# Optimization experiments

Measured on AMD Instinct MI355X. Metric: run time of the kernel, lower is better.

The kernel has to match this reference:

```python
import jax, jax.numpy as jnp
import numpy as np

B, T, C, H = 8, 1024, 1024, 16
Dh = C // H
EPS = 1e-5


def layernorm(x, g, b):
    m = jnp.mean(x, axis=-1, keepdims=True)
    v = jnp.mean((x - m) ** 2, axis=-1, keepdims=True)
    return g * (x - m) / jnp.sqrt(v + EPS) + b


def setup_inputs() -> dict:
    key = jax.random.key(0)
    ks = jax.random.split(key, 10)
    s = 0.02
    return {
        "x": jax.random.normal(ks[0], (B, T, C), jnp.float32),
        "Wq": jax.random.normal(ks[1], (H, C, Dh), jnp.float32) * s,
        "Wk": jax.random.normal(ks[2], (H, C, Dh), jnp.float32) * s,
        "Wv": jax.random.normal(ks[3], (H, C, Dh), jnp.float32) * s,
        "Wproj": jax.random.normal(ks[4], (C, C), jnp.float32) * s,
        "bproj": jnp.zeros((C,), jnp.float32),
        "W1": jax.random.normal(ks[5], (C, C), jnp.float32) * s,
        "b1": jnp.zeros((C,), jnp.float32),
        "W2": jax.random.normal(ks[6], (C, C), jnp.float32) * s,
        "b2": jnp.zeros((C,), jnp.float32),
        "g1": jnp.ones((C,), jnp.float32),
        "beta1": jnp.zeros((C,), jnp.float32),
        "g2": jnp.ones((C,), jnp.float32),
        "beta2": jnp.zeros((C,), jnp.float32),
    }


def reference(x, Wq, Wk, Wv, Wproj, bproj, W1, b1, W2, b2, g1, beta1, g2, beta2):
    # pre-LN multi-head causal self-attention + residual
    xn = layernorm(x, g1, beta1)
    q = jnp.einsum("btc,hcd->bhtd", xn, Wq)
    k = jnp.einsum("btc,hcd->bhtd", xn, Wk)
    v = jnp.einsum("btc,hcd->bhtd", xn, Wv)
    scores = jnp.einsum("bhtd,bhsd->bhts", q, k) * (Dh ** -0.5)
    causal = jnp.tril(jnp.ones((T, T), bool))  # [T,T]
    scores = jnp.where(causal, scores, -jnp.inf)
    wei = jax.nn.softmax(scores, axis=-1)
    attn = jnp.einsum("bhts,bhsd->bhtd", wei, v)
    attn = attn.transpose(0, 2, 1, 3).reshape(B, T, C)  # concat heads
    x = x + attn @ Wproj + bproj
    # pre-LN MLP (n_emb -> n_emb, ReLU, n_emb -> n_emb) + residual
    xn2 = layernorm(x, g2, beta2)
    h = jax.nn.relu(xn2 @ W1 + b1)
    x = x + h @ W2 + b2
    return x
```

## Files before the change

kernel.cpp:

```cpp
#include <hip/hip_runtime.h>
#include <hip/hip_bf16.h>

#define KDIM 1024

typedef __bf16  bf16x8  __attribute__((ext_vector_type(8)));
typedef float   floatx4 __attribute__((ext_vector_type(4)));

__device__ inline short f2bf(float f) {
    unsigned u = __float_as_uint(f);
    u += 0x7fffu + ((u >> 16) & 1u);
    return (short)(u >> 16);
}
__device__ inline float bf2f(short s) {
    return __uint_as_float(((unsigned)(unsigned short)s) << 16);
}

__device__ inline floatx4 mfma16(bf16x8 a, bf16x8 b, floatx4 c) {
    return __builtin_amdgcn_mfma_f32_16x16x32_bf16(a, b, c, 0, 0, 0);
}

__device__ inline void load_lds16(const void* g, void* l) {
    __builtin_amdgcn_global_load_lds(
        (__attribute__((address_space(1))) void*)(unsigned long long)g,
        (__attribute__((address_space(3))) void*)(unsigned)(unsigned long long)l,
        16, 0, 0);
}

template <bool BF16IN>
__global__ __launch_bounds__(256) void ln_kernel(
    const void* __restrict__ xv, const float* __restrict__ g,
    const float* __restrict__ be, short* __restrict__ out)
{
    const int row = blockIdx.x, tid = threadIdx.x;
    float4 v;
    if constexpr (BF16IN) {
        const short4 s4 = ((const short4*)xv)[(size_t)row * 256 + tid];
        v.x = bf2f(s4.x); v.y = bf2f(s4.y); v.z = bf2f(s4.z); v.w = bf2f(s4.w);
    } else {
        v = ((const float4*)xv)[(size_t)row * 256 + tid];
    }
    float s  = v.x + v.y + v.z + v.w;
    float s2 = v.x * v.x + v.y * v.y + v.z * v.z + v.w * v.w;
    #pragma unroll
    for (int off = 32; off; off >>= 1) {
        s  += __shfl_down(s, off);
        s2 += __shfl_down(s2, off);
    }
    __shared__ float red1[4], red2[4];
    const int w = tid >> 6, lane = tid & 63;
    if (lane == 0) { red1[w] = s; red2[w] = s2; }
    __syncthreads();
    s  = red1[0] + red1[1] + red1[2] + red1[3];
    s2 = red2[0] + red2[1] + red2[2] + red2[3];
    const float mean = s * (1.0f / 1024.0f);
    const float var  = s2 * (1.0f / 1024.0f) - mean * mean;
    const float rstd = rsqrtf(var + 1e-5f);
    const float4 gg = ((const float4*)g)[tid];
    const float4 bb = ((const float4*)be)[tid];
    short4 o;
    o.x = f2bf((v.x - mean) * rstd * gg.x + bb.x);
    o.y = f2bf((v.y - mean) * rstd * gg.y + bb.y);
    o.z = f2bf((v.z - mean) * rstd * gg.z + bb.z);
    o.w = f2bf((v.w - mean) * rstd * gg.w + bb.w);
    *(short4*)(out + (size_t)row * 1024 + tid * 4) = o;
}

__global__ void pack_qkvT(const float* __restrict__ Wq, const float* __restrict__ Wk,
                          const float* __restrict__ Wv, short* __restrict__ dst)
{
    __shared__ float tile[32][33];
    const int n0 = blockIdx.x * 32, c0 = blockIdx.y * 32;
    const int tx = threadIdx.x, ty = threadIdx.y;
    const int grp = n0 >> 10;
    const float* W = (grp == 0) ? Wq : (grp == 1 ? Wk : Wv);
    const int nb = n0 & 1023, hh = nb >> 6, d0 = nb & 63;
    #pragma unroll
    for (int j = 0; j < 32; j += 8)
        tile[ty + j][tx] = W[hh * 65536 + (c0 + ty + j) * 64 + d0 + tx];
    __syncthreads();
    #pragma unroll
    for (int j = 0; j < 32; j += 8)
        dst[(size_t)(n0 + ty + j) * 1024 + c0 + tx] = f2bf(tile[tx][ty + j]);
}

__global__ void packT(const float* __restrict__ src, short* __restrict__ dst)
{
    __shared__ float tile[32][33];
    const int n0 = blockIdx.x * 32, k0 = blockIdx.y * 32;
    const int tx = threadIdx.x, ty = threadIdx.y;
    #pragma unroll
    for (int j = 0; j < 32; j += 8)
        tile[ty + j][tx] = src[(size_t)(k0 + ty + j) * 1024 + n0 + tx];
    __syncthreads();
    #pragma unroll
    for (int j = 0; j < 32; j += 8)
        dst[(size_t)(n0 + ty + j) * 1024 + k0 + tx] = f2bf(tile[tx][ty + j]);
}

template <int EPI, bool SWAP>
__global__ __launch_bounds__(256) void gemm_bt(
    const short* __restrict__ A, const short* __restrict__ BT, int N,
    const float* __restrict__ bias, const float* __restrict__ residF,
    const short* __restrict__ residH,
    float* __restrict__ outF, short* __restrict__ outH,
    short* __restrict__ qO, short* __restrict__ kO, short* __restrict__ vtO)
{
    const int tid = threadIdx.x, lane = tid & 63, w = tid >> 6;
    const int wm = w >> 1, wn = w & 1;
    const int mi = lane & 15, quad = lane >> 4;
    const int lid = blockIdx.x + gridDim.x * blockIdx.y;
    const int xcd = lid & 7, i8 = lid >> 3;
    const int rowBase = (xcd * 8 + (i8 & 7)) * 128;
    const int colBase = (i8 >> 3) * 128;

    __shared__ alignas(16) short As[128 * 64];
    __shared__ alignas(16) short Bs[128 * 64];

    const floatx4 z4 = {0.f, 0.f, 0.f, 0.f};
    floatx4 acc[4][4];
    #pragma unroll
    for (int i = 0; i < 4; ++i)
        #pragma unroll
        for (int j = 0; j < 4; ++j) acc[i][j] = z4;

    for (int k0 = 0; k0 < KDIM; k0 += 64) {
        __syncthreads();
        #pragma unroll
        for (int i = 0; i < 4; ++i) {
            const int cb = i * 256 + w * 64;
            const int chunk = cb + lane;
            const int r = chunk >> 3, c = chunk & 7;
            const int csw = c ^ (r & 7);
            load_lds16(A  + (size_t)(rowBase + r) * KDIM + k0 + csw * 8, (char*)As + cb * 16);
            load_lds16(BT + (size_t)(colBase + r) * KDIM + k0 + csw * 8, (char*)Bs + cb * 16);
        }
        __syncthreads();
        #pragma unroll
        for (int kh = 0; kh < 2; ++kh) {
            bf16x8 af[4], bfv[4];
            #pragma unroll
            for (int it = 0; it < 4; ++it) {
                const int ra = wm * 64 + it * 16 + mi;
                af[it] = *(const bf16x8*)(As + (ra * 8 + ((kh * 4 + quad) ^ (ra & 7))) * 8);
            }
            #pragma unroll
            for (int jt = 0; jt < 4; ++jt) {
                const int rb = wn * 64 + jt * 16 + mi;
                bfv[jt] = *(const bf16x8*)(Bs + (rb * 8 + ((kh * 4 + quad) ^ (rb & 7))) * 8);
            }
            #pragma unroll
            for (int it = 0; it < 4; ++it)
                #pragma unroll
                for (int jt = 0; jt < 4; ++jt) {
                    if constexpr (SWAP)
                        acc[it][jt] = mfma16(bfv[jt], af[it], acc[it][jt]);
                    else
                        acc[it][jt] = mfma16(af[it], bfv[jt], acc[it][jt]);
                }
        }
    }

    if constexpr (SWAP) {
        #pragma unroll
        for (int it = 0; it < 4; ++it) {
            const int row = rowBase + wm * 64 + it * 16 + mi;
            #pragma unroll
            for (int jt = 0; jt < 4; ++jt) {
                const int col0 = colBase + wn * 64 + jt * 16 + quad * 4;
                const floatx4 a4 = acc[it][jt];
                if constexpr (EPI == 0) {
                    if (colBase < 1024) {
                        short4 o;
                        o.x = f2bf(a4[0] * 0.125f); o.y = f2bf(a4[1] * 0.125f);
                        o.z = f2bf(a4[2] * 0.125f); o.w = f2bf(a4[3] * 0.125f);
                        *(short4*)(qO + (size_t)row * 1024 + col0) = o;
                    } else {
                        short4 o;
                        o.x = f2bf(a4[0]); o.y = f2bf(a4[1]);
                        o.z = f2bf(a4[2]); o.w = f2bf(a4[3]);
                        *(short4*)(kO + (size_t)row * 1024 + (col0 - 1024)) = o;
                    }
                } else if constexpr (EPI == 2) {
                    const float4 b4 = *(const float4*)(bias + col0);
                    short4 o;
                    o.x = f2bf(fmaxf(a4[0] + b4.x, 0.f));
                    o.y = f2bf(fmaxf(a4[1] + b4.y, 0.f));
                    o.z = f2bf(fmaxf(a4[2] + b4.z, 0.f));
                    o.w = f2bf(fmaxf(a4[3] + b4.w, 0.f));
                    *(short4*)(outH + (size_t)row * N + col0) = o;
                } else if constexpr (EPI == 4) {
                    const float4 b4 = *(const float4*)(bias + col0);
                    const float4 r4 = *(const float4*)(residF + (size_t)row * N + col0);
                    short4 o;
                    o.x = f2bf(a4[0] + b4.x + r4.x);
                    o.y = f2bf(a4[1] + b4.y + r4.y);
                    o.z = f2bf(a4[2] + b4.z + r4.z);
                    o.w = f2bf(a4[3] + b4.w + r4.w);
                    *(short4*)(outH + (size_t)row * N + col0) = o;
                } else {
                    const float4 b4 = *(const float4*)(bias + col0);
                    const short4 r4 = *(const short4*)(residH + (size_t)row * N + col0);
                    float4 o;
                    o.x = a4[0] + b4.x + bf2f(r4.x);
                    o.y = a4[1] + b4.y + bf2f(r4.y);
                    o.z = a4[2] + b4.z + bf2f(r4.z);
                    o.w = a4[3] + b4.w + bf2f(r4.w);
                    *(float4*)(outF + (size_t)row * N + col0) = o;
                }
            }
        }
    } else {
        #pragma unroll
        for (int it = 0; it < 4; ++it) {
            const int row0 = rowBase + wm * 64 + it * 16 + quad * 4;
            const int bb = row0 >> 10, t0 = row0 & 1023;
            #pragma unroll
            for (int jt = 0; jt < 4; ++jt) {
                const int c = colBase + wn * 64 + jt * 16 + mi;
                const floatx4 a4 = acc[it][jt];
                short4 o;
                o.x = f2bf(a4[0]); o.y = f2bf(a4[1]);
                o.z = f2bf(a4[2]); o.w = f2bf(a4[3]);
                *(short4*)(vtO + ((size_t)bb << 20) + ((size_t)c << 10) + t0) = o;
            }
        }
    }
}

#define PSTR 88
__device__ __forceinline__ void attn_qk_pv(
    const bf16x8 qf0, const bf16x8 qf1,
    floatx4 (&o)[4], float (&lsum)[4],
    const short* Ks, const short* Vs, short* myP,
    const int mi, const int quad, const int kq, const int diagRowOff)
{
    const floatx4 z4 = {0.f, 0.f, 0.f, 0.f};
    const bool diag = diagRowOff >= 0;
    floatx4 sa[4];
    #pragma unroll
    for (int j = 0; j < 4; ++j) {
        const int row = j * 16 + mi;
        const int sw = row & 7;
        floatx4 s4 = z4;
        s4 = mfma16(qf0, *(const bf16x8*)(Ks + row * 64 + ((quad ^ sw) << 3)), s4);
        s4 = mfma16(qf1, *(const bf16x8*)(Ks + row * 64 + (((quad + 4) ^ sw) << 3)), s4);
        sa[j] = s4;
    }
    #pragma unroll
    for (int j = 0; j < 4; ++j)
        #pragma unroll
        for (int r = 0; r < 4; ++r) {
            float p = __expf(sa[j][r]);
            if (diag && (j * 16 + mi > diagRowOff + quad * 4 + r)) p = 0.f;
            lsum[r] += p;
            myP[(quad * 4 + r) * PSTR + j * 16 + mi] = f2bf(p);
        }
    __asm__ volatile("s_waitcnt lgkmcnt(0)" ::: "memory");
    const bf16x8 pf0 = *(const bf16x8*)(myP + mi * PSTR + kq);
    const bf16x8 pf1 = *(const bf16x8*)(myP + mi * PSTR + 32 + kq);
    #pragma unroll
    for (int d = 0; d < 4; ++d) {
        const int row = d * 16 + mi;
        const int sw = row & 7;
        o[d] = mfma16(pf0, *(const bf16x8*)(Vs + row * 64 + ((quad ^ sw) << 3)), o[d]);
        o[d] = mfma16(pf1, *(const bf16x8*)(Vs + row * 64 + (((quad + 4) ^ sw) << 3)), o[d]);
    }
}

__global__ __launch_bounds__(256, 4) void flash_attn(
    const short* __restrict__ Q, const short* __restrict__ K,
    const short* __restrict__ Vt, short* __restrict__ O)
{
    const int tid = threadIdx.x, lane = tid & 63, w = tid >> 6;
    const int mi = lane & 15, quad = lane >> 4, kq = quad * 8;
    const int lid = blockIdx.x;
    const int xcd = lid & 7, i8 = lid >> 3;
    const int bh = xcd * 16 + (i8 & 15);
    const int pi = i8 >> 4;
    const int h = bh & 15, b = bh >> 4;
    const int tA = pi, tB = 15 - pi;
    const int qbA = tA * 64, qbB = tB * 64;

    __shared__ alignas(16) short Ks[64 * 64];
    __shared__ alignas(16) short Vs[64 * 64];
    __shared__ alignas(16) short Ps[4][16 * PSTR];

    const size_t qoffA = ((size_t)(b * 1024 + qbA + w * 16 + mi)) * 1024 + h * 64;
    const size_t qoffB = ((size_t)(b * 1024 + qbB + w * 16 + mi)) * 1024 + h * 64;
    const bf16x8 qA0 = *(const bf16x8*)(Q + qoffA + kq);
    const bf16x8 qA1 = *(const bf16x8*)(Q + qoffA + 32 + kq);
    const bf16x8 qB0 = *(const bf16x8*)(Q + qoffB + kq);
    const bf16x8 qB1 = *(const bf16x8*)(Q + qoffB + 32 + kq);

    const floatx4 z4 = {0.f, 0.f, 0.f, 0.f};
    floatx4 oA[4], oB[4];
    float lA[4], lB[4];
    #pragma unroll
    for (int i = 0; i < 4; ++i) { oA[i] = z4; oB[i] = z4; lA[i] = 0.f; lB[i] = 0.f; }

    short* myP = &Ps[w][0];
    for (int t = 0; t <= tB; ++t) {
        const int s0 = t * 64;
        __syncthreads();
        #pragma unroll
        for (int i = 0; i < 2; ++i) {
            const int cb = i * 256 + w * 64;
            const int chunk = cb + lane;
            const int r = chunk >> 3, c = chunk & 7;
            const int csw = c ^ (r & 7);
            load_lds16(K + ((size_t)(b * 1024 + s0 + r)) * 1024 + h * 64 + csw * 8,
                       (char*)Ks + cb * 16);
            load_lds16(Vt + ((size_t)b << 20) + ((size_t)(h * 64 + r) << 10) + s0 + csw * 8,
                       (char*)Vs + cb * 16);
        }
        __syncthreads();

        if (t <= tA)
            attn_qk_pv(qA0, qA1, oA, lA, Ks, Vs, myP, mi, quad, kq,
                       (t == tA) ? (w * 16) : -1);
        attn_qk_pv(qB0, qB1, oB, lB, Ks, Vs, myP, mi, quad, kq,
                   (t == tB) ? (w * 16) : -1);
    }

    #pragma unroll
    for (int r = 0; r < 4; ++r) {
        float sA = lA[r], sB = lB[r];
        #pragma unroll
        for (int off = 1; off < 16; off <<= 1) {
            sA += __shfl_xor(sA, off);
            sB += __shfl_xor(sB, off);
        }
        lA[r] = 1.0f / sA;
        lB[r] = 1.0f / sB;
    }
    #pragma unroll
    for (int d = 0; d < 4; ++d)
        #pragma unroll
        for (int r = 0; r < 4; ++r) {
            const int col = h * 64 + d * 16 + mi;
            const int rowA = b * 1024 + qbA + w * 16 + quad * 4 + r;
            const int rowB = b * 1024 + qbB + w * 16 + quad * 4 + r;
            O[(size_t)rowA * 1024 + col] = f2bf(oA[d][r] * lA[r]);
            O[(size_t)rowB * 1024 + col] = f2bf(oB[d][r] * lB[r]);
        }
}

extern "C" void kernel_launch(void* const* d_in, const int* in_sizes, int n_in,
                              void* d_out, int out_size, void* d_ws, size_t ws_size,
                              hipStream_t stream)
{
    (void)in_sizes; (void)n_in; (void)out_size; (void)ws_size;
    const float* x     = (const float*)d_in[0];
    const float* Wq    = (const float*)d_in[1];
    const float* Wk    = (const float*)d_in[2];
    const float* Wv    = (const float*)d_in[3];
    const float* Wproj = (const float*)d_in[4];
    const float* bproj = (const float*)d_in[5];
    const float* W1    = (const float*)d_in[6];
    const float* b1    = (const float*)d_in[7];
    const float* W2    = (const float*)d_in[8];
    const float* b2    = (const float*)d_in[9];
    const float* g1    = (const float*)d_in[10];
    const float* be1   = (const float*)d_in[11];
    const float* g2    = (const float*)d_in[12];
    const float* be2   = (const float*)d_in[13];
    float* out = (float*)d_out;

    char* ws = (char*)d_ws;
    const size_t MB = 1u << 20;
    short* Qb     = (short*)(ws + 0 * MB);
    short* Kb     = (short*)(ws + 16 * MB);
    short* Vtb    = (short*)(ws + 32 * MB);
    short* XN     = (short*)(ws + 48 * MB);
    short* AT     = (short*)(ws + 64 * MB);
    short* R2b    = (short*)(ws + 80 * MB);
    short* WqkvT  = (short*)(ws + 112 * MB);
    short* WprojT = (short*)(ws + 118 * MB);
    short* W1T    = (short*)(ws + 120 * MB);
    short* W2T    = (short*)(ws + 122 * MB);

    const dim3 tb(32, 8);
    pack_qkvT<<<dim3(96, 32), tb, 0, stream>>>(Wq, Wk, Wv, WqkvT);
    packT<<<dim3(32, 32), tb, 0, stream>>>(Wproj, WprojT);
    packT<<<dim3(32, 32), tb, 0, stream>>>(W1, W1T);
    packT<<<dim3(32, 32), tb, 0, stream>>>(W2, W2T);

    ln_kernel<false><<<8192, 256, 0, stream>>>(x, g1, be1, XN);

    gemm_bt<0, true><<<dim3(16, 64), 256, 0, stream>>>(XN, WqkvT, 1024,
        nullptr, nullptr, nullptr, nullptr, nullptr, Qb, Kb, nullptr);
    gemm_bt<3, false><<<dim3(8, 64), 256, 0, stream>>>(XN, WqkvT + 2048 * KDIM, 1024,
        nullptr, nullptr, nullptr, nullptr, nullptr, nullptr, nullptr, Vtb);

    flash_attn<<<1024, 256, 0, stream>>>(Qb, Kb, Vtb, AT);

    gemm_bt<4, true><<<dim3(8, 64), 256, 0, stream>>>(AT, WprojT, 1024,
        bproj, x, nullptr, nullptr, R2b, nullptr, nullptr, nullptr);

    ln_kernel<true><<<8192, 256, 0, stream>>>(R2b, g2, be2, XN);

    gemm_bt<2, true><<<dim3(8, 64), 256, 0, stream>>>(XN, W1T, 1024,
        b1, nullptr, nullptr, nullptr, AT, nullptr, nullptr, nullptr);

    gemm_bt<5, true><<<dim3(8, 64), 256, 0, stream>>>(AT, W2T, 1024,
        b2, nullptr, R2b, out, nullptr, nullptr, nullptr, nullptr);
}
```

Measured before the change: 326.7 us.

## Double-buffer GEMM K-loop, template tile height, merge weight pack kernels

Measured after the change: 337.4 us. 1.03x slower.

```diff
diff --git a/kernel.cpp b/kernel.cpp
--- a/kernel.cpp
+++ b/kernel.cpp
@@ -65,105 +65,129 @@
     *(short4*)(out + (size_t)row * 1024 + tid * 4) = o;
 }
 
-__global__ void pack_qkvT(const float* __restrict__ Wq, const float* __restrict__ Wk,
-                          const float* __restrict__ Wv, short* __restrict__ dst)
+__global__ void pack_all(const float* __restrict__ Wq, const float* __restrict__ Wk,
+                         const float* __restrict__ Wv, const float* __restrict__ Wproj,
+                         const float* __restrict__ W1, const float* __restrict__ W2,
+                         short* __restrict__ qkvT, short* __restrict__ projT,
+                         short* __restrict__ w1T, short* __restrict__ w2T)
 {
     __shared__ float tile[32][33];
-    const int n0 = blockIdx.x * 32, c0 = blockIdx.y * 32;
+    const int bx = blockIdx.x, c0 = blockIdx.y * 32;
     const int tx = threadIdx.x, ty = threadIdx.y;
-    const int grp = n0 >> 10;
-    const float* W = (grp == 0) ? Wq : (grp == 1 ? Wk : Wv);
-    const int nb = n0 & 1023, hh = nb >> 6, d0 = nb & 63;
-    #pragma unroll
-    for (int j = 0; j < 32; j += 8)
-        tile[ty + j][tx] = W[hh * 65536 + (c0 + ty + j) * 64 + d0 + tx];
-    __syncthreads();
-    #pragma unroll
-    for (int j = 0; j < 32; j += 8)
-        dst[(size_t)(n0 + ty + j) * 1024 + c0 + tx] = f2bf(tile[tx][ty + j]);
-}
-
-__global__ void packT(const float* __restrict__ src, short* __restrict__ dst)
-{
-    __shared__ float tile[32][33];
-    const int n0 = blockIdx.x * 32, k0 = blockIdx.y * 32;
-    const int tx = threadIdx.x, ty = threadIdx.y;
-    #pragma unroll
-    for (int j = 0; j < 32; j += 8)
-        tile[ty + j][tx] = src[(size_t)(k0 + ty + j) * 1024 + n0 + tx];
-    __syncthreads();
-    #pragma unroll
-    for (int j = 0; j < 32; j += 8)
-        dst[(size_t)(n0 + ty + j) * 1024 + k0 + tx] = f2bf(tile[tx][ty + j]);
-}
-
-template <int EPI, bool SWAP>
-__global__ __launch_bounds__(256) void gemm_bt(
+    if (bx < 96) {
+        const int n0 = bx * 32;
+        const int grp = n0 >> 10;
+        const float* W = (grp == 0) ? Wq : (grp == 1 ? Wk : Wv);
+        const int nb = n0 & 1023, hh = nb >> 6, d0 = nb & 63;
+        #pragma unroll
+        for (int j = 0; j < 32; j += 8)
+            tile[ty + j][tx] = W[hh * 65536 + (c0 + ty + j) * 64 + d0 + tx];
+        __syncthreads();
+        #pragma unroll
+        for (int j = 0; j < 32; j += 8)
+            qkvT[(size_t)(n0 + ty + j) * 1024 + c0 + tx] = f2bf(tile[tx][ty + j]);
+    } else {
+        const int which = (bx - 96) >> 5;
+        const int n0 = ((bx - 96) & 31) * 32;
+        const float* src = (which == 0) ? Wproj : (which == 1 ? W1 : W2);
+        short* dst = (which == 0) ? projT : (which == 1 ? w1T : w2T);
+        #pragma unroll
+        for (int j = 0; j < 32; j += 8)
+            tile[ty + j][tx] = src[(size_t)(c0 + ty + j) * 1024 + n0 + tx];
+        __syncthreads();
+        #pragma unroll
+        for (int j = 0; j < 32; j += 8)
+            dst[(size_t)(n0 + ty + j) * 1024 + c0 + tx] = f2bf(tile[tx][ty + j]);
+    }
+}
+
+template <int EPI, bool SWAP, int TM>
+__global__ __launch_bounds__(256, 4) void gemm_bt(
     const short* __restrict__ A, const short* __restrict__ BT, int N,
     const float* __restrict__ bias, const float* __restrict__ residF,
     const short* __restrict__ residH,
     float* __restrict__ outF, short* __restrict__ outH,
     short* __restrict__ qO, short* __restrict__ kO, short* __restrict__ vtO)
 {
+    constexpr int IT = TM / 32;
+    constexpr int PP = (8192 / TM) / 8;
     const int tid = threadIdx.x, lane = tid & 63, w = tid >> 6;
     const int wm = w >> 1, wn = w & 1;
     const int mi = lane & 15, quad = lane >> 4;
     const int lid = blockIdx.x + gridDim.x * blockIdx.y;
     const int xcd = lid & 7, i8 = lid >> 3;
-    const int rowBase = (xcd * 8 + (i8 & 7)) * 128;
-    const int colBase = (i8 >> 3) * 128;
-
-    __shared__ alignas(16) short As[128 * 64];
-    __shared__ alignas(16) short Bs[128 * 64];
+    const int rowBase = (xcd * PP + (i8 % PP)) * TM;
+    const int colBase = (i8 / PP) * 128;
+
+    __shared__ alignas(16) short As[2][TM * 32];
+    __shared__ alignas(16) short Bs[2][128 * 32];
 
     const floatx4 z4 = {0.f, 0.f, 0.f, 0.f};
-    floatx4 acc[4][4];
-    #pragma unroll
-    for (int i = 0; i < 4; ++i)
+    floatx4 acc[IT][4];
+    #pragma unroll
+    for (int i = 0; i < IT; ++i)
         #pragma unroll
         for (int j = 0; j < 4; ++j) acc[i][j] = z4;
 
-    for (int k0 = 0; k0 < KDIM; k0 += 64) {
-        __syncthreads();
-        #pragma unroll
-        for (int i = 0; i < 4; ++i) {
+    auto stage = [&](int k0, int buf) {
+        #pragma unroll
+        for (int i = 0; i < TM / 64; ++i) {
             const int cb = i * 256 + w * 64;
             const int chunk = cb + lane;
-            const int r = chunk >> 3, c = chunk & 7;
-            const int csw = c ^ (r & 7);
-            load_lds16(A  + (size_t)(rowBase + r) * KDIM + k0 + csw * 8, (char*)As + cb * 16);
-            load_lds16(BT + (size_t)(colBase + r) * KDIM + k0 + csw * 8, (char*)Bs + cb * 16);
-        }
-        __syncthreads();
-        #pragma unroll
-        for (int kh = 0; kh < 2; ++kh) {
-            bf16x8 af[4], bfv[4];
-            #pragma unroll
-            for (int it = 0; it < 4; ++it) {
-                const int ra = wm * 64 + it * 16 + mi;
-                af[it] = *(const bf16x8*)(As + (ra * 8 + ((kh * 4 + quad) ^ (ra & 7))) * 8);
-            }
+            const int r = chunk >> 2, cc = chunk & 3;
+            const int csw = cc ^ ((r >> 1) & 3);
+            load_lds16(A + (size_t)(rowBase + r) * KDIM + k0 + csw * 8,
+                       (char*)As[buf] + cb * 16);
+        }
+        #pragma unroll
+        for (int i = 0; i < 2; ++i) {
+            const int cb = i * 256 + w * 64;
+            const int chunk = cb + lane;
+            const int r = chunk >> 2, cc = chunk & 3;
+            const int csw = cc ^ ((r >> 1) & 3);
+            load_lds16(BT + (size_t)(colBase + r) * KDIM + k0 + csw * 8,
+                       (char*)Bs[buf] + cb * 16);
+        }
+    };
+
+    auto compute = [&](const short* Ac, const short* Bc) {
+        bf16x8 af[IT], bfv[4];
+        #pragma unroll
+        for (int it = 0; it < IT; ++it) {
+            const int ra = wm * (TM / 2) + it * 16 + mi;
+            af[it] = *(const bf16x8*)(Ac + ra * 32 + ((quad ^ ((ra >> 1) & 3)) << 3));
+        }
+        #pragma unroll
+        for (int jt = 0; jt < 4; ++jt) {
+            const int rb = wn * 64 + jt * 16 + mi;
+            bfv[jt] = *(const bf16x8*)(Bc + rb * 32 + ((quad ^ ((rb >> 1) & 3)) << 3));
+        }
+        #pragma unroll
+        for (int it = 0; it < IT; ++it)
             #pragma unroll
             for (int jt = 0; jt < 4; ++jt) {
-                const int rb = wn * 64 + jt * 16 + mi;
-                bfv[jt] = *(const bf16x8*)(Bs + (rb * 8 + ((kh * 4 + quad) ^ (rb & 7))) * 8);
+                if constexpr (SWAP)
+                    acc[it][jt] = mfma16(bfv[jt], af[it], acc[it][jt]);
+                else
+                    acc[it][jt] = mfma16(af[it], bfv[jt], acc[it][jt]);
             }
-            #pragma unroll
-            for (int it = 0; it < 4; ++it)
-                #pragma unroll
-                for (int jt = 0; jt < 4; ++jt) {
-                    if constexpr (SWAP)
-                        acc[it][jt] = mfma16(bfv[jt], af[it], acc[it][jt]);
-                    else
-                        acc[it][jt] = mfma16(af[it], bfv[jt], acc[it][jt]);
-                }
-        }
+    };
+
+    stage(0, 0);
+    #pragma unroll 1
+    for (int c = 0; c < KDIM / 32; c += 2) {
+        __syncthreads();
+        if (c + 1 < KDIM / 32) stage((c + 1) * 32, 1);
+        compute(As[0], Bs[0]);
+        __syncthreads();
+        if (c + 2 < KDIM / 32) stage((c + 2) * 32, 0);
+        compute(As[1], Bs[1]);
     }
 
     if constexpr (SWAP) {
         #pragma unroll
-        for (int it = 0; it < 4; ++it) {
-            const int row = rowBase + wm * 64 + it * 16 + mi;
+        for (int it = 0; it < IT; ++it) {
+            const int row = rowBase + wm * (TM / 2) + it * 16 + mi;
             #pragma unroll
             for (int jt = 0; jt < 4; ++jt) {
                 const int col0 = colBase + wn * 64 + jt * 16 + quad * 4;
@@ -211,8 +235,8 @@
         }
     } else {
         #pragma unroll
-        for (int it = 0; it < 4; ++it) {
-            const int row0 = rowBase + wm * 64 + it * 16 + quad * 4;
+        for (int it = 0; it < IT; ++it) {
+            const int row0 = rowBase + wm * (TM / 2) + it * 16 + quad * 4;
             const int bb = row0 >> 10, t0 = row0 & 1023;
             #pragma unroll
             for (int jt = 0; jt < 4; ++jt) {
@@ -379,29 +403,26 @@
     short* W1T    = (short*)(ws + 120 * MB);
     short* W2T    = (short*)(ws + 122 * MB);
 
-    const dim3 tb(32, 8);
-    pack_qkvT<<<dim3(96, 32), tb, 0, stream>>>(Wq, Wk, Wv, WqkvT);
-    packT<<<dim3(32, 32), tb, 0, stream>>>(Wproj, WprojT);
-    packT<<<dim3(32, 32), tb, 0, stream>>>(W1, W1T);
-    packT<<<dim3(32, 32), tb, 0, stream>>>(W2, W2T);
+    pack_all<<<dim3(192, 32), dim3(32, 8), 0, stream>>>(
+        Wq, Wk, Wv, Wproj, W1, W2, WqkvT, WprojT, W1T, W2T);
 
     ln_kernel<false><<<8192, 256, 0, stream>>>(x, g1, be1, XN);
 
-    gemm_bt<0, true><<<dim3(16, 64), 256, 0, stream>>>(XN, WqkvT, 1024,
+    gemm_bt<0, true, 128><<<dim3(16, 64), 256, 0, stream>>>(XN, WqkvT, 1024,
         nullptr, nullptr, nullptr, nullptr, nullptr, Qb, Kb, nullptr);
-    gemm_bt<3, false><<<dim3(8, 64), 256, 0, stream>>>(XN, WqkvT + 2048 * KDIM, 1024,
+    gemm_bt<3, false, 64><<<dim3(8, 128), 256, 0, stream>>>(XN, WqkvT + 2048 * KDIM, 1024,
         nullptr, nullptr, nullptr, nullptr, nullptr, nullptr, nullptr, Vtb);
 
     flash_attn<<<1024, 256, 0, stream>>>(Qb, Kb, Vtb, AT);
 
-    gemm_bt<4, true><<<dim3(8, 64), 256, 0, stream>>>(AT, WprojT, 1024,
+    gemm_bt<4, true, 64><<<dim3(8, 128), 256, 0, stream>>>(AT, WprojT, 1024,
         bproj, x, nullptr, nullptr, R2b, nullptr, nullptr, nullptr);
 
     ln_kernel<true><<<8192, 256, 0, stream>>>(R2b, g2, be2, XN);
 
-    gemm_bt<2, true><<<dim3(8, 64), 256, 0, stream>>>(XN, W1T, 1024,
+    gemm_bt<2, true, 64><<<dim3(8, 128), 256, 0, stream>>>(XN, W1T, 1024,
         b1, nullptr, nullptr, nullptr, AT, nullptr, nullptr, nullptr);
 
-    gemm_bt<5, true><<<dim3(8, 64), 256, 0, stream>>>(AT, W2T, 1024,
+    gemm_bt<5, true, 64><<<dim3(8, 128), 256, 0, stream>>>(AT, W2T, 1024,
         b2, nullptr, R2b, out, nullptr, nullptr, nullptr, nullptr);
 }
```
